# Kernel tuning notes

Measured on AMD Instinct MI355X. Metric: run time of the kernel, lower is better.

## Reference

```python
import jax, jax.numpy as jnp
import numpy as np
from scipy.special import binom

NSTATES = 4
DEG = 3
NINPUTS = NSTATES + 1  # statedependent*nstates + timedependent
N_DATA = 1_000_000


def _gen_exponents(ninputs, deg):
    """Replay the source module's recursive monomial enumeration exactly
    (same DFS order) so feature columns line up with the torch version."""
    idx_list = []

    def loop_rec(idx_array, n):
        for i in range(ninputs):
            idx_copy = idx_array.copy()
            idx_copy[i] += 1
            if idx_copy not in idx_list:
                idx_list.append(idx_copy)
            if n > 0:
                loop_rec(idx_copy, n - 1)

    loop_rec([0] * ninputs, deg - 1)
    return np.asarray(idx_list, dtype=np.int32)  # (pol_terms, ninputs)


def setup_inputs() -> dict:
    key = jax.random.key(0)
    k_x, k_t, k_l, k_o, k_f = jax.random.split(key, 5)
    pol_terms = int(binom(NINPUTS + DEG, DEG) - 1)  # 55
    n_terms = pol_terms + 2 * NINPUTS               # 65
    E = jnp.asarray(_gen_exponents(NINPUTS, DEG))   # (55, 5) int32
    return {
        "x": jax.random.normal(k_x, (N_DATA, NSTATES), dtype=jnp.float32),
        "t": jax.random.uniform(k_t, (N_DATA, 1), dtype=jnp.float32),
        "layer": jax.random.normal(k_l, (n_terms,), dtype=jnp.float32),
        "omegas": jax.random.normal(k_o, (2 * NINPUTS,), dtype=jnp.float32),
        "ext_filter": jax.random.normal(k_f, (1, 2), dtype=jnp.float32),
        "E": E,
    }


def reference(x, t, layer, omegas, ext_filter, E):
    xt = jnp.concatenate([x, t], axis=-1)          # (N, ninputs)
    n_in = xt.shape[1]
    # Polynomial library: monomial k = prod_j xt[:, j] ** E[k, j].
    # Loop is over the small fixed ninputs dim; avoids (N, K, ninputs) blowup.
    feat = xt[:, 0][:, None] ** E[None, :, 0]      # (N, pol_terms)
    for j in range(1, n_in):
        feat = feat * (xt[:, j][:, None] ** E[None, :, j])
    # Trig library (source uses only omegas[0] and omegas[1]).
    cosx = jnp.cos(omegas[0] * xt)                 # (N, ninputs)
    sinx = jnp.sin(omegas[1] * xt)                 # (N, ninputs)
    features = jnp.concatenate([feat, cosx, sinx], axis=1)  # (N, n_terms)
    s = jnp.sum(layer * features, axis=1, keepdims=True)    # (N, 1)
    return s @ ext_filter                           # (N, 2)
```

## Files before the change

### kernel.cpp

```cpp
#include <hip/hip_runtime.h>

#define NIN 5
#define POL 55

__global__ void prep_kernel(const float* __restrict__ layer,
                            const float* __restrict__ omegas,
                            const float* __restrict__ ext_filter,
                            const int* __restrict__ E,
                            float* __restrict__ w) {
    int k = threadIdx.x;
    if (k < POL) {
        int e[NIN], d = 0;
        #pragma unroll
        for (int j = 0; j < NIN; ++j) { e[j] = E[k * NIN + j]; d += e[j]; }
        int vars[3] = {0, 0, 0};
        int c = 0;
        for (int j = 0; j < NIN; ++j)
            for (int r = 0; r < e[j]; ++r) vars[c++] = j;
        int slot;
        if (d == 1) {
            slot = vars[0];
        } else if (d == 2) {
            int j = vars[0], kk = vars[1];
            slot = 5 + j * NIN - j * (j - 1) / 2 + (kk - j);
        } else {
            const int base3[5] = {0, 15, 25, 31, 34};
            int j = vars[0], kk = vars[1], l = vars[2];
            int m = NIN - j;
            int a = kk - j;
            slot = 20 + base3[j] + a * m - a * (a - 1) / 2 + (l - kk);
        }
        w[slot] = layer[k];
    } else if (k < POL + 10) {
        w[k] = layer[k];
    } else if (k == POL + 10) {
        w[65] = omegas[0];
        w[66] = omegas[1];
        w[67] = ext_filter[0];
        w[68] = ext_filter[1];
    }
}

__global__ __launch_bounds__(256) void main_kernel(
    const float4* __restrict__ x,
    const float* __restrict__ t,
    const float* __restrict__ w,
    float2* __restrict__ out,
    int n) {
    int i = blockIdx.x * blockDim.x + threadIdx.x;
    if (i >= n) return;

    float4 xv = x[i];
    float tv = t[i];
    float v[NIN] = {xv.x, xv.y, xv.z, xv.w, tv};

    float s = 0.f;
    int i2 = 5, i3 = 20;
    #pragma unroll
    for (int j = 0; j < NIN; ++j) {
        float qj = 0.f;
        #pragma unroll
        for (int k = j; k < NIN; ++k) {
            float r = w[i2++];
            #pragma unroll
            for (int l = k; l < NIN; ++l) r = fmaf(w[i3++], v[l], r);
            qj = fmaf(r, v[k], qj);
        }
        s = fmaf(v[j], w[j] + qj, s);
    }

    float w0 = w[65], w1 = w[66];
    #pragma unroll
    for (int j = 0; j < NIN; ++j) {
        s = fmaf(w[55 + j], __cosf(w0 * v[j]), s);
        s = fmaf(w[60 + j], __sinf(w1 * v[j]), s);
    }

    out[i] = make_float2(s * w[67], s * w[68]);
}

extern "C" void kernel_launch(void* const* d_in, const int* in_sizes, int n_in,
                              void* d_out, int out_size, void* d_ws, size_t ws_size,
                              hipStream_t stream) {
    const float* x          = (const float*)d_in[0];
    const float* t          = (const float*)d_in[1];
    const float* layer      = (const float*)d_in[2];
    const float* omegas     = (const float*)d_in[3];
    const float* ext_filter = (const float*)d_in[4];
    const int*   E          = (const int*)d_in[5];
    float* w = (float*)d_ws;

    int n = in_sizes[0] / 4;

    prep_kernel<<<1, 128, 0, stream>>>(layer, omegas, ext_filter, E, w);
    main_kernel<<<(n + 255) / 256, 256, 0, stream>>>(
        (const float4*)x, t, w, (float2*)d_out, n);
}
```

Before: 81.19 us.

## Fuse weight prep into main kernel and process four rows per thread

Merges the single-block prep kernel into the main kernel: each block rebuilds the permuted weight table in shared memory and then synchronizes. Each thread now handles four rows, reading t as float4 and writing outputs as two float4 stores, so there are fewer threads and the memory accesses are wider. This removes one kernel launch and the serial dependency on the prep kernel. In exchange, every block repeats the prep work and reads E. The code assumes N is divisible by 4 and has no tail handling.

```diff
diff --git a/kernel.cpp b/kernel.cpp
--- a/kernel.cpp
+++ b/kernel.cpp
@@ -3,14 +3,20 @@
 #define NIN 5
 #define POL 55
 
-__global__ void prep_kernel(const float* __restrict__ layer,
-                            const float* __restrict__ omegas,
-                            const float* __restrict__ ext_filter,
-                            const int* __restrict__ E,
-                            float* __restrict__ w) {
+__global__ __launch_bounds__(256) void fused_kernel(
+    const float4* __restrict__ x,
+    const float4* __restrict__ t4,
+    const float* __restrict__ layer,
+    const float* __restrict__ omegas,
+    const float* __restrict__ ext_filter,
+    const int* __restrict__ E,
+    float4* __restrict__ out4,
+    int n4) {
+    __shared__ float w[69];
     int k = threadIdx.x;
     if (k < POL) {
-        int e[NIN], d = 0;
+        int e[NIN];
+        int d = 0;
         #pragma unroll
         for (int j = 0; j < NIN; ++j) { e[j] = E[k * NIN + j]; d += e[j]; }
         int vars[3] = {0, 0, 0};
@@ -39,44 +45,47 @@
         w[67] = ext_filter[0];
         w[68] = ext_filter[1];
     }
-}
+    __syncthreads();
 
-__global__ __launch_bounds__(256) void main_kernel(
-    const float4* __restrict__ x,
-    const float* __restrict__ t,
-    const float* __restrict__ w,
-    float2* __restrict__ out,
-    int n) {
     int i = blockIdx.x * blockDim.x + threadIdx.x;
-    if (i >= n) return;
+    if (i >= n4) return;
 
-    float4 xv = x[i];
-    float tv = t[i];
-    float v[NIN] = {xv.x, xv.y, xv.z, xv.w, tv};
+    float4 tv = t4[i];
+    float ts[4] = {tv.x, tv.y, tv.z, tv.w};
+    float w0 = w[65], w1 = w[66];
+    float f0 = w[67], f1 = w[68];
+    float res[4];
 
-    float s = 0.f;
-    int i2 = 5, i3 = 20;
     #pragma unroll
-    for (int j = 0; j < NIN; ++j) {
-        float qj = 0.f;
+    for (int r = 0; r < 4; ++r) {
+        float4 xv = x[i * 4 + r];
+        float v[NIN] = {xv.x, xv.y, xv.z, xv.w, ts[r]};
+
+        float s = 0.f;
+        int i2 = 5, i3 = 20;
         #pragma unroll
-        for (int k = j; k < NIN; ++k) {
-            float r = w[i2++];
+        for (int j = 0; j < NIN; ++j) {
+            float qj = 0.f;
             #pragma unroll
-            for (int l = k; l < NIN; ++l) r = fmaf(w[i3++], v[l], r);
-            qj = fmaf(r, v[k], qj);
+            for (int kk = j; kk < NIN; ++kk) {
+                float rr = w[i2++];
+                #pragma unroll
+                for (int l = kk; l < NIN; ++l) rr = fmaf(w[i3++], v[l], rr);
+                qj = fmaf(rr, v[kk], qj);
+            }
+            s = fmaf(v[j], w[j] + qj, s);
         }
-        s = fmaf(v[j], w[j] + qj, s);
+
+        #pragma unroll
+        for (int j = 0; j < NIN; ++j) {
+            s = fmaf(w[55 + j], __cosf(w0 * v[j]), s);
+            s = fmaf(w[60 + j], __sinf(w1 * v[j]), s);
+        }
+        res[r] = s;
     }
 
-    float w0 = w[65], w1 = w[66];
-    #pragma unroll
-    for (int j = 0; j < NIN; ++j) {
-        s = fmaf(w[55 + j], __cosf(w0 * v[j]), s);
-        s = fmaf(w[60 + j], __sinf(w1 * v[j]), s);
-    }
-
-    out[i] = make_float2(s * w[67], s * w[68]);
+    out4[2 * i]     = make_float4(res[0] * f0, res[0] * f1, res[1] * f0, res[1] * f1);
+    out4[2 * i + 1] = make_float4(res[2] * f0, res[2] * f1, res[3] * f0, res[3] * f1);
 }
 
 extern "C" void kernel_launch(void* const* d_in, const int* in_sizes, int n_in,
@@ -88,11 +97,11 @@
     const float* omegas     = (const float*)d_in[3];
     const float* ext_filter = (const float*)d_in[4];
     const int*   E          = (const int*)d_in[5];
-    float* w = (float*)d_ws;
 
-    int n = in_sizes[0] / 4;
+    int n = in_sizes[1];
+    int n4 = n / 4;
 
-    prep_kernel<<<1, 128, 0, stream>>>(layer, omegas, ext_filter, E, w);
-    main_kernel<<<(n + 255) / 256, 256, 0, stream>>>(
-        (const float4*)x, t, w, (float2*)d_out, n);
+    fused_kernel<<<(n4 + 255) / 256, 256, 0, stream>>>(
+        (const float4*)x, (const float4*)t, layer, omegas, ext_filter, E,
+        (float4*)d_out, n4);
 }
```

New measurement: 79.70 us. Within noise of the previous version (-1.8%).
